# Kernel optimization log

Hardware: AMD Instinct MI355X
Metric: run time of the kernel (lower is better)

## Reference

```python
import jax, jax.numpy as jnp
import numpy as np

N, Z_DIM, HID = 2048, 64, 64

def setup_inputs() -> dict:
    key = jax.random.key(0)
    k_z, k_w1, k_w2 = jax.random.split(key, 3)
    # Kaiming-ish scales for realism
    z = jax.random.normal(k_z, (N, Z_DIM), dtype=jnp.float32)
    W1 = jax.random.normal(k_w1, (2 * Z_DIM, HID), dtype=jnp.float32) * (1.0 / np.sqrt(2 * Z_DIM))
    b1 = jnp.zeros((HID,), dtype=jnp.float32)
    W2 = jax.random.normal(k_w2, (HID, 1), dtype=jnp.float32) * (1.0 / np.sqrt(HID))
    b2 = jnp.zeros((1,), dtype=jnp.float32)
    return {"z": z, "W1": W1, "b1": b1, "W2": W2, "b2": b2}

def reference(z, W1, b1, W2, b2):
    # Linear(cat([zi, zj])) == zi @ W1[:z_dim] + zj @ W1[z_dim:] + b1
    # (same math as torch's concat, without materializing the (N,N,2*z_dim) tensor)
    zd = z.shape[1]
    pi = z @ W1[:zd]   # (N, hid) contribution of row node i
    pj = z @ W1[zd:]   # (N, hid) contribution of col node j
    h = jax.nn.relu(pi[:, None, :] + pj[None, :, :] + b1)  # (N, N, hid)
    logits = (h @ W2)[..., 0] + b2[0]                       # (N, N)
    return jax.nn.sigmoid(logits)
```

## Files before the change

### kernel.cpp

```cpp
#include <hip/hip_runtime.h>

#define N 2048
#define ZD 64

typedef float f32x4 __attribute__((ext_vector_type(4)));
typedef float f32x2 __attribute__((ext_vector_type(2)));


__global__ __launch_bounds__(256) void edge_proj(
    const float* __restrict__ z, const float* __restrict__ W1,
    const float* __restrict__ b1, const float* __restrict__ W2,
    float* __restrict__ pT)
{
    const int t = threadIdx.x;
    const int i = blockIdx.x * 64 + (t & 63);
    const int colg = t >> 6;
    const int col0 = blockIdx.y * 8 + colg * 2;

    float zr[ZD];
    const f32x4* zrow = (const f32x4*)(z + i * ZD);
    #pragma unroll
    for (int q = 0; q < ZD / 4; ++q) {
        f32x4 v = zrow[q];
        zr[q * 4 + 0] = v[0]; zr[q * 4 + 1] = v[1];
        zr[q * 4 + 2] = v[2]; zr[q * 4 + 3] = v[3];
    }

    float acc[2];
    #pragma unroll
    for (int cc = 0; cc < 2; ++cc) {
        const int col = __builtin_amdgcn_readfirstlane(col0 + cc);
        const float* w1c = (col < 64) ? (W1 + col) : (W1 + 64 * 64 + (col - 64));
        float a = (col < 64) ? b1[col] : 0.0f;
        #pragma unroll
        for (int d = 0; d < ZD; ++d)
            a = fmaf(zr[d], w1c[d * 64], a);
        acc[cc] = a;
        pT[(col0 + cc) * N + i] = a;
    }

    float part = 0.0f;
    #pragma unroll
    for (int cc = 0; cc < 2; ++cc) {
        const int col = __builtin_amdgcn_readfirstlane(col0 + cc);
        part = fmaf(acc[cc], W2[col & 63], part);
    }
    float* rp = pT + 128 * N;
    const int p = blockIdx.y * 4 + colg;
    rp[p * N + i] = part;
}

__global__ __launch_bounds__(256) void edge_main2(
    const float* __restrict__ pT, const float* __restrict__ W2,
    const float* __restrict__ b2, float* __restrict__ out)
{
    __shared__ float ash[64][64];
    __shared__ float bsh[64][128];
    __shared__ float w2s[64];
    __shared__ float ris[64];
    __shared__ float rjs[128];

    const int t = threadIdx.x;
    const int i0 = blockIdx.y * 64;
    const int j0 = blockIdx.x * 128;
    const float* rp = pT + 128 * N;

    {
        #pragma unroll
        for (int rep = 0; rep < 4; ++rep) {
            const int cidx = rep * 256 + t;
            const int k = cidx >> 4, c4 = (cidx & 15) << 2;
            *(f32x4*)&ash[k][c4] = *(const f32x4*)(pT + k * N + i0 + c4);
        }
        #pragma unroll
        for (int rep = 0; rep < 8; ++rep) {
            const int cidx = rep * 256 + t;
            const int k = cidx >> 5, c4 = (cidx & 31) << 2;
            *(f32x4*)&bsh[k][c4] = *(const f32x4*)(pT + (64 + k) * N + j0 + c4);
        }
        if (t < 64) {
            float s = 0.0f;
            #pragma unroll
            for (int p = 0; p < 32; ++p) s += rp[p * N + i0 + t];
            ris[t] = s;
        } else if (t < 192) {
            float s = 0.0f;
            #pragma unroll
            for (int p = 32; p < 64; ++p) s += rp[p * N + j0 + (t - 64)];
            rjs[t - 64] = s;
        } else {
            w2s[t - 192] = W2[t - 192];
        }
    }
    __syncthreads();

    const int tx = t & 15, ty = t >> 4;
    float acc[4][8];
    #pragma unroll
    for (int r = 0; r < 4; ++r)
        #pragma unroll
        for (int c = 0; c < 8; ++c) acc[r][c] = 0.0f;

    #pragma unroll 4
    for (int k4 = 0; k4 < 64; k4 += 4) {
        f32x4 wv = *(const f32x4*)&w2s[k4];
        #pragma unroll
        for (int kk = 0; kk < 4; ++kk) {
            const int k = k4 + kk;
            f32x4 av  = *(const f32x4*)&ash[k][ty * 4];
            f32x4 bv0 = *(const f32x4*)&bsh[k][tx * 4];
            f32x4 bv1 = *(const f32x4*)&bsh[k][64 + tx * 4];
            const float w = wv[kk];
            #pragma unroll
            for (int r = 0; r < 4; ++r) {
                f32x2 ar = { av[r], av[r] };
                #pragma unroll
                for (int c2 = 0; c2 < 2; ++c2) {
                    f32x2 b01 = { bv0[c2 * 2], bv0[c2 * 2 + 1] };
                    f32x2 t01 = ar + b01;
                    acc[r][c2 * 2]     = fmaf(fabsf(t01[0]), w, acc[r][c2 * 2]);
                    acc[r][c2 * 2 + 1] = fmaf(fabsf(t01[1]), w, acc[r][c2 * 2 + 1]);
                    f32x2 b23 = { bv1[c2 * 2], bv1[c2 * 2 + 1] };
                    f32x2 t23 = ar + b23;
                    acc[r][c2 * 2 + 4] = fmaf(fabsf(t23[0]), w, acc[r][c2 * 2 + 4]);
                    acc[r][c2 * 2 + 5] = fmaf(fabsf(t23[1]), w, acc[r][c2 * 2 + 5]);
                }
            }
        }
    }

    const float C = -0.72134752f;
    const float base = -1.44269504f * b2[0];
    float riC[4], rjC[8];
    #pragma unroll
    for (int r = 0; r < 4; ++r) riC[r] = fmaf(ris[ty * 4 + r], C, base);
    #pragma unroll
    for (int c = 0; c < 4; ++c) {
        rjC[c]     = rjs[tx * 4 + c] * C;
        rjC[c + 4] = rjs[64 + tx * 4 + c] * C;
    }

    #pragma unroll
    for (int r = 0; r < 4; ++r) {
        f32x4 o0, o1;
        #pragma unroll
        for (int c = 0; c < 4; ++c) {
            float x0 = fmaf(acc[r][c],     C, riC[r] + rjC[c]);
            float x1 = fmaf(acc[r][c + 4], C, riC[r] + rjC[c + 4]);
            o0[c] = __builtin_amdgcn_rcpf(1.0f + __builtin_amdgcn_exp2f(x0));
            o1[c] = __builtin_amdgcn_rcpf(1.0f + __builtin_amdgcn_exp2f(x1));
        }
        float* orow = out + (i0 + ty * 4 + r) * N + j0 + tx * 4;
        __builtin_nontemporal_store(o0, (f32x4*)orow);
        __builtin_nontemporal_store(o1, (f32x4*)(orow + 64));
    }
}

extern "C" void kernel_launch(void* const* d_in, const int* in_sizes, int n_in,
                              void* d_out, int out_size, void* d_ws, size_t ws_size,
                              hipStream_t stream) {
    const float* z  = (const float*)d_in[0];
    const float* W1 = (const float*)d_in[1];
    const float* b1 = (const float*)d_in[2];
    const float* W2 = (const float*)d_in[3];
    const float* b2 = (const float*)d_in[4];
    float* out = (float*)d_out;
    float* pT  = (float*)d_ws;

    edge_proj<<<dim3(N / 64, 16), 256, 0, stream>>>(z, W1, b1, W2, pT);
    edge_main2<<<dim3(N / 128, N / 64), 256, 0, stream>>>(pT, W2, b2, out);
}
```

Baseline: 90.64 us.

## Fuse projection into main kernel, recomputing per-tile node projections in LDS

Drops the separate projection kernel and its global workspace. Each tile block now computes its own 64 row and 128 column projections of z through W1 directly into shared memory, along with the W2-weighted partial sums. This removes one kernel launch and a global write/read round trip. The cost is redundant work: each node's projection is recomputed by every block that shares its row or column tile, adding about 64x128x... FMAs per block and extra register pressure.

New measurement: 103.6 us. 1.14x slower.

```diff
diff --git a/kernel.cpp b/kernel.cpp
--- a/kernel.cpp
+++ b/kernel.cpp
@@ -6,52 +6,9 @@
 typedef float f32x4 __attribute__((ext_vector_type(4)));
 typedef float f32x2 __attribute__((ext_vector_type(2)));
 
-
-__global__ __launch_bounds__(256) void edge_proj(
+__global__ __launch_bounds__(256) void edge_fused(
     const float* __restrict__ z, const float* __restrict__ W1,
     const float* __restrict__ b1, const float* __restrict__ W2,
-    float* __restrict__ pT)
-{
-    const int t = threadIdx.x;
-    const int i = blockIdx.x * 64 + (t & 63);
-    const int colg = t >> 6;
-    const int col0 = blockIdx.y * 8 + colg * 2;
-
-    float zr[ZD];
-    const f32x4* zrow = (const f32x4*)(z + i * ZD);
-    #pragma unroll
-    for (int q = 0; q < ZD / 4; ++q) {
-        f32x4 v = zrow[q];
-        zr[q * 4 + 0] = v[0]; zr[q * 4 + 1] = v[1];
-        zr[q * 4 + 2] = v[2]; zr[q * 4 + 3] = v[3];
-    }
-
-    float acc[2];
-    #pragma unroll
-    for (int cc = 0; cc < 2; ++cc) {
-        const int col = __builtin_amdgcn_readfirstlane(col0 + cc);
-        const float* w1c = (col < 64) ? (W1 + col) : (W1 + 64 * 64 + (col - 64));
-        float a = (col < 64) ? b1[col] : 0.0f;
-        #pragma unroll
-        for (int d = 0; d < ZD; ++d)
-            a = fmaf(zr[d], w1c[d * 64], a);
-        acc[cc] = a;
-        pT[(col0 + cc) * N + i] = a;
-    }
-
-    float part = 0.0f;
-    #pragma unroll
-    for (int cc = 0; cc < 2; ++cc) {
-        const int col = __builtin_amdgcn_readfirstlane(col0 + cc);
-        part = fmaf(acc[cc], W2[col & 63], part);
-    }
-    float* rp = pT + 128 * N;
-    const int p = blockIdx.y * 4 + colg;
-    rp[p * N + i] = part;
-}
-
-__global__ __launch_bounds__(256) void edge_main2(
-    const float* __restrict__ pT, const float* __restrict__ W2,
     const float* __restrict__ b2, float* __restrict__ out)
 {
     __shared__ float ash[64][64];
@@ -59,39 +16,75 @@
     __shared__ float w2s[64];
     __shared__ float ris[64];
     __shared__ float rjs[128];
+    __shared__ float rip[4][64];
+    __shared__ float rjp[2][128];
 
     const int t = threadIdx.x;
     const int i0 = blockIdx.y * 64;
     const int j0 = blockIdx.x * 128;
-    const float* rp = pT + 128 * N;
 
     {
+        const int li = t & 63;
+        const int colbase = __builtin_amdgcn_readfirstlane(t >> 6) << 4;
+        const f32x4* zrow = (const f32x4*)(z + (i0 + li) * ZD);
+        float a[16];
         #pragma unroll
-        for (int rep = 0; rep < 4; ++rep) {
-            const int cidx = rep * 256 + t;
-            const int k = cidx >> 4, c4 = (cidx & 15) << 2;
-            *(f32x4*)&ash[k][c4] = *(const f32x4*)(pT + k * N + i0 + c4);
+        for (int cc = 0; cc < 16; ++cc) a[cc] = b1[colbase + cc];
+        #pragma unroll 4
+        for (int dq = 0; dq < 16; ++dq) {
+            f32x4 zv = zrow[dq];
+            #pragma unroll
+            for (int dd = 0; dd < 4; ++dd) {
+                const int d = dq * 4 + dd;
+                const float zd = zv[dd];
+                const float* w1r = W1 + d * 64 + colbase;
+                #pragma unroll
+                for (int cc = 0; cc < 16; ++cc)
+                    a[cc] = fmaf(zd, w1r[cc], a[cc]);
+            }
         }
+        float part = 0.0f;
         #pragma unroll
-        for (int rep = 0; rep < 8; ++rep) {
-            const int cidx = rep * 256 + t;
-            const int k = cidx >> 5, c4 = (cidx & 31) << 2;
-            *(f32x4*)&bsh[k][c4] = *(const f32x4*)(pT + (64 + k) * N + j0 + c4);
+        for (int cc = 0; cc < 16; ++cc) {
+            ash[colbase + cc][li] = a[cc];
+            part = fmaf(a[cc], W2[colbase + cc], part);
         }
-        if (t < 64) {
-            float s = 0.0f;
+        rip[colbase >> 4][li] = part;
+    }
+
+    {
+        const int lj = t & 127;
+        const int qbase = __builtin_amdgcn_readfirstlane(t >> 7) << 5;
+        const f32x4* zrow = (const f32x4*)(z + (j0 + lj) * ZD);
+        float a[32];
+        #pragma unroll
+        for (int cc = 0; cc < 32; ++cc) a[cc] = 0.0f;
+        #pragma unroll 4
+        for (int dq = 0; dq < 16; ++dq) {
+            f32x4 zv = zrow[dq];
             #pragma unroll
-            for (int p = 0; p < 32; ++p) s += rp[p * N + i0 + t];
-            ris[t] = s;
-        } else if (t < 192) {
-            float s = 0.0f;
-            #pragma unroll
-            for (int p = 32; p < 64; ++p) s += rp[p * N + j0 + (t - 64)];
-            rjs[t - 64] = s;
-        } else {
-            w2s[t - 192] = W2[t - 192];
+            for (int dd = 0; dd < 4; ++dd) {
+                const int d = dq * 4 + dd;
+                const float zd = zv[dd];
+                const float* w1r = W1 + (64 + d) * 64 + qbase;
+                #pragma unroll
+                for (int cc = 0; cc < 32; ++cc)
+                    a[cc] = fmaf(zd, w1r[cc], a[cc]);
+            }
         }
+        float part = 0.0f;
+        #pragma unroll
+        for (int cc = 0; cc < 32; ++cc) {
+            bsh[qbase + cc][lj] = a[cc];
+            part = fmaf(a[cc], W2[qbase + cc], part);
+        }
+        rjp[qbase >> 5][lj] = part;
     }
+    if (t >= 192) w2s[t - 192] = W2[t - 192];
+    __syncthreads();
+
+    if (t < 64)       ris[t] = ((rip[0][t] + rip[1][t]) + rip[2][t]) + rip[3][t];
+    else if (t < 192) rjs[t - 64] = rjp[0][t - 64] + rjp[1][t - 64];
     __syncthreads();
 
     const int tx = t & 15, ty = t >> 4;
@@ -165,8 +158,7 @@
     const float* W2 = (const float*)d_in[3];
     const float* b2 = (const float*)d_in[4];
     float* out = (float*)d_out;
-    float* pT  = (float*)d_ws;
+    (void)d_ws; (void)ws_size;
 
-    edge_proj<<<dim3(N / 64, 16), 256, 0, stream>>>(z, W1, b1, W2, pT);
-    edge_main2<<<dim3(N / 128, N / 64), 256, 0, stream>>>(pT, W2, b2, out);
+    edge_fused<<<dim3(N / 128, N / 64), 256, 0, stream>>>(z, W1, b1, W2, b2, out);
 }
```

## Split hidden-dim reduction across two thread groups with LDS partial-sum combine

Applied to the files above, without the earlier changes.

Doubles the block to 512 threads and splits the 64-wide hidden reduction into two halves of 32, one per 256-thread group. The second group writes its partial accumulators into the reused B tile in shared memory, and the first group adds them before the sigmoid epilogue. The aim is more waves per CU and a shorter serial inner loop per thread. The cost is an extra barrier, an LDS round-trip of partial sums, and half the threads sitting idle during the epilogue.

Measured after the change: 93.61 us. 1.03x slower.

```diff
diff --git a/kernel.cpp b/kernel.cpp
--- a/kernel.cpp
+++ b/kernel.cpp
@@ -50,7 +50,7 @@
     rp[p * N + i] = part;
 }
 
-__global__ __launch_bounds__(256) void edge_main2(
+__global__ __launch_bounds__(512) void edge_main2(
     const float* __restrict__ pT, const float* __restrict__ W2,
     const float* __restrict__ b2, float* __restrict__ out)
 {
@@ -67,14 +67,14 @@
 
     {
         #pragma unroll
-        for (int rep = 0; rep < 4; ++rep) {
-            const int cidx = rep * 256 + t;
+        for (int rep = 0; rep < 2; ++rep) {
+            const int cidx = rep * 512 + t;
             const int k = cidx >> 4, c4 = (cidx & 15) << 2;
             *(f32x4*)&ash[k][c4] = *(const f32x4*)(pT + k * N + i0 + c4);
         }
         #pragma unroll
-        for (int rep = 0; rep < 8; ++rep) {
-            const int cidx = rep * 256 + t;
+        for (int rep = 0; rep < 4; ++rep) {
+            const int cidx = rep * 512 + t;
             const int k = cidx >> 5, c4 = (cidx & 31) << 2;
             *(f32x4*)&bsh[k][c4] = *(const f32x4*)(pT + (64 + k) * N + j0 + c4);
         }
@@ -88,13 +88,16 @@
             #pragma unroll
             for (int p = 32; p < 64; ++p) s += rp[p * N + j0 + (t - 64)];
             rjs[t - 64] = s;
-        } else {
+        } else if (t < 256) {
             w2s[t - 192] = W2[t - 192];
         }
     }
     __syncthreads();
 
-    const int tx = t & 15, ty = t >> 4;
+    const int g  = t >> 8;
+    const int tt = t & 255;
+    const int tx = tt & 15, ty = tt >> 4;
+    const int kbase = g << 5;
     float acc[4][8];
     #pragma unroll
     for (int r = 0; r < 4; ++r)
@@ -102,11 +105,11 @@
         for (int c = 0; c < 8; ++c) acc[r][c] = 0.0f;
 
     #pragma unroll 4
-    for (int k4 = 0; k4 < 64; k4 += 4) {
-        f32x4 wv = *(const f32x4*)&w2s[k4];
+    for (int k4 = 0; k4 < 32; k4 += 4) {
+        f32x4 wv = *(const f32x4*)&w2s[kbase + k4];
         #pragma unroll
         for (int kk = 0; kk < 4; ++kk) {
-            const int k = k4 + kk;
+            const int k = kbase + k4 + kk;
             f32x4 av  = *(const f32x4*)&ash[k][ty * 4];
             f32x4 bv0 = *(const f32x4*)&bsh[k][tx * 4];
             f32x4 bv1 = *(const f32x4*)&bsh[k][64 + tx * 4];
@@ -128,6 +131,30 @@
             }
         }
     }
+
+    __syncthreads();
+
+    float* pacc = &bsh[0][0];
+    if (g == 1) {
+        #pragma unroll
+        for (int r = 0; r < 4; ++r)
+            #pragma unroll
+            for (int c2 = 0; c2 < 4; ++c2) {
+                f32x2 v = { acc[r][c2 * 2], acc[r][c2 * 2 + 1] };
+                *(f32x2*)&pacc[((r * 4 + c2) * 256 + tt) * 2] = v;
+            }
+    }
+    __syncthreads();
+    if (g == 1) return;
+
+    #pragma unroll
+    for (int r = 0; r < 4; ++r)
+        #pragma unroll
+        for (int c2 = 0; c2 < 4; ++c2) {
+            f32x2 v = *(const f32x2*)&pacc[((r * 4 + c2) * 256 + tt) * 2];
+            acc[r][c2 * 2]     += v[0];
+            acc[r][c2 * 2 + 1] += v[1];
+        }
 
     const float C = -0.72134752f;
     const float base = -1.44269504f * b2[0];
@@ -168,5 +195,5 @@
     float* pT  = (float*)d_ws;
 
     edge_proj<<<dim3(N / 64, 16), 256, 0, stream>>>(z, W1, b1, W2, pT);
-    edge_main2<<<dim3(N / 128, N / 64), 256, 0, stream>>>(pT, W2, b2, out);
+    edge_main2<<<dim3(N / 128, N / 64), 512, 0, stream>>>(pT, W2, b2, out);
 }
```
